# Optimization experiments

Hardware: AMD Instinct MI355X
Metric: run time of the kernel (lower is better)

Reference implementation:

```python
import jax, jax.numpy as jnp
import numpy as np

B, L, D = 32768, 256, 16  # batch, chain length, bond dim; physical dim d=2


def setup_inputs() -> dict:
    key = jax.random.key(0)
    k_phi, k_first, k_mid, k_last = jax.random.split(key, 4)
    scale = 1.0 / np.sqrt(2.0 * D)  # variance-preserving chain
    phi_batch = jax.random.normal(k_phi, (B, L, 2), dtype=jnp.float32)
    core_first = jax.random.normal(k_first, (2, D), dtype=jnp.float32) * scale
    cores_mid = jax.random.normal(k_mid, (L - 2, D, 2, D), dtype=jnp.float32) * scale
    core_last = jax.random.normal(k_last, (D, 2), dtype=jnp.float32) * scale
    out_bias = jnp.zeros((), dtype=jnp.float32)
    return {
        "phi_batch": phi_batch,
        "core_first": core_first,
        "cores_mid": cores_mid,
        "core_last": core_last,
        "out_bias": out_bias,
    }


def reference(phi_batch, core_first, cores_mid, core_last, out_bias):
    # MPS / tensor-train contraction, batched over samples.
    # Each sample contracts feature vectors phi[i] (len-2) into the physical
    # index of core i, then chains the resulting D x D matrices via a
    # left-to-right bond-space matvec (what cotengra would find per-sample).
    # v0: [B, D] = phi[:,0] contracted with first core [2, D]
    v0 = jnp.einsum("bp,pd->bd", phi_batch[:, 0], core_first)

    # middle features, scan-major layout: [L-2, B, 2]
    phis_mid = jnp.swapaxes(phi_batch[:, 1:-1], 0, 1)

    def step(v, xs):
        phi_t, core = xs  # phi_t: [B, 2], core: [D, 2, D]
        # contract bond then physical index; never materialize [B, D, D]
        u = jnp.einsum("bq,qpr->bpr", v, core)   # [B, 2, D]
        v_new = jnp.einsum("bp,bpr->br", phi_t, u)  # [B, D]
        return v_new, None

    v, _ = jax.lax.scan(step, v0, (phis_mid, cores_mid))

    # close the chain with last core [D, 2] and last feature [B, 2]
    out = jnp.einsum("bq,qp,bp->b", v, core_last, phi_batch[:, -1])
    return out + out_bias
```

## Files before the change

### kernel.cpp

```cpp
#include <hip/hip_runtime.h>
#include <stdint.h>


typedef short  bf16x8 __attribute__((ext_vector_type(8)));
typedef float  f32x4  __attribute__((ext_vector_type(4)));
typedef int    i32x4  __attribute__((ext_vector_type(4)));
typedef unsigned int u32;

#define NPF 64
#define NPB 63
#define BWD_OFF (NPF*4*64)

#define PACK_HI(hi, lo) ((int)__builtin_amdgcn_perm((u32)(hi), (u32)(lo), 0x07060302u))

__device__ __forceinline__ u32 rne_bump(u32 u){ return u + 0x7FFFu + ((u >> 16) & 1u); }

__global__ void build_pair_frags(const float* __restrict__ cm, i32x4* __restrict__ ws)
{
  __shared__ float Ca[512], Cb[512];
  const int bid = blockIdx.x;
  const bool fwd = bid < NPF;
  const int j  = fwd ? bid : bid - NPF;
  const int ta = fwd ? 2*j     : 252 - 2*j;
  const int tb = fwd ? 2*j + 1 : 253 - 2*j;
  {
    const float* A = cm + ta*512;
    const float* B = cm + tb*512;
    for (int i = threadIdx.x; i < 512; i += 256){ Ca[i] = A[i]; Cb[i] = B[i]; }
  }
  __syncthreads();
  const int f    = threadIdx.x >> 6;
  const int lane = threadIdx.x & 63;
  const int m    = lane & 15;
  const int g    = lane >> 4;
  const int p    = f >> 1, q = f & 1;
  u32 hi[4], lo[4];
  #pragma unroll
  for (int x = 0; x < 4; ++x){
    const int cq = 4*g + x;
    float acc = 0.f;
    #pragma unroll
    for (int r = 0; r < 16; ++r){
      const float a = fwd ? Ca[cq*32 + p*16 + r] : Ca[m*32 + p*16 + r];
      const float b = fwd ? Cb[r*32 + q*16 + m]  : Cb[r*32 + q*16 + cq];
      acc = fmaf(a, b, acc);
    }
    const u32 u  = __float_as_uint(acc);
    const u32 aa = rne_bump(u);
    const float hf = __uint_as_float(aa & 0xFFFF0000u);
    const u32 bb = rne_bump(__float_as_uint(acc - hf));
    hi[x] = aa >> 16; lo[x] = bb >> 16;
  }
  i32x4 w;
  w[0] = (int)(hi[0] | (hi[1] << 16));
  w[1] = (int)(hi[2] | (hi[3] << 16));
  w[2] = (int)(lo[0] | (lo[1] << 16));
  w[3] = (int)(lo[2] | (lo[3] << 16));
  ws[(fwd ? 0 : BWD_OFF) + (j*4 + f)*64 + lane] = w;
}

__device__ __forceinline__ void make_bfrag(const float (&v)[4], i32x4 &bfr)
{
  const u32 u0 = __float_as_uint(v[0]), u1 = __float_as_uint(v[1]);
  const u32 u2 = __float_as_uint(v[2]), u3 = __float_as_uint(v[3]);
  const float l0 = v[0] - __uint_as_float(u0 & 0xFFFF0000u);
  const float l1 = v[1] - __uint_as_float(u1 & 0xFFFF0000u);
  const float l2 = v[2] - __uint_as_float(u2 & 0xFFFF0000u);
  const float l3 = v[3] - __uint_as_float(u3 & 0xFFFF0000u);
  bfr[0] = PACK_HI(u1, u0);
  bfr[1] = PACK_HI(u3, u2);
  bfr[2] = PACK_HI(__float_as_uint(l1), __float_as_uint(l0));
  bfr[3] = PACK_HI(__float_as_uint(l3), __float_as_uint(l2));
}

__device__ __forceinline__ void pair_step(
    const i32x4 &G0, const i32x4 &G1, const i32x4 &G2, const i32x4 &G3,
    float2 cA, float2 cB, float (&v)[4], i32x4 &bfr)
{
  const float c00 = cA.x*cB.x, c01 = cA.x*cB.y;
  const float c10 = cA.y*cB.x, c11 = cA.y*cB.y;
  i32x4 sw; sw[0]=bfr[2]; sw[1]=bfr[3]; sw[2]=bfr[0]; sw[3]=bfr[1];
  const bf16x8 bh = __builtin_bit_cast(bf16x8, bfr);
  const bf16x8 bs = __builtin_bit_cast(bf16x8, sw);
  const f32x4 z = {0.f,0.f,0.f,0.f};
  f32x4 a00 = __builtin_amdgcn_mfma_f32_16x16x32_bf16(__builtin_bit_cast(bf16x8,G0), bh, z, 0,0,0);
  a00 = __builtin_amdgcn_mfma_f32_16x16x32_bf16(__builtin_bit_cast(bf16x8,G0), bs, a00, 0,0,0);
  f32x4 a01 = __builtin_amdgcn_mfma_f32_16x16x32_bf16(__builtin_bit_cast(bf16x8,G1), bh, z, 0,0,0);
  a01 = __builtin_amdgcn_mfma_f32_16x16x32_bf16(__builtin_bit_cast(bf16x8,G1), bs, a01, 0,0,0);
  f32x4 a10 = __builtin_amdgcn_mfma_f32_16x16x32_bf16(__builtin_bit_cast(bf16x8,G2), bh, z, 0,0,0);
  a10 = __builtin_amdgcn_mfma_f32_16x16x32_bf16(__builtin_bit_cast(bf16x8,G2), bs, a10, 0,0,0);
  f32x4 a11 = __builtin_amdgcn_mfma_f32_16x16x32_bf16(__builtin_bit_cast(bf16x8,G3), bh, z, 0,0,0);
  a11 = __builtin_amdgcn_mfma_f32_16x16x32_bf16(__builtin_bit_cast(bf16x8,G3), bs, a11, 0,0,0);
  #pragma unroll
  for (int i2 = 0; i2 < 4; ++i2)
    v[i2] = c00*a00[i2] + c01*a01[i2] + c10*a10[i2] + c11*a11[i2];
  make_bfrag(v, bfr);
}

__global__ __launch_bounds__(256, 2) void mps_chain(
  const float* __restrict__ phi,
  const float* __restrict__ core_first,
  const float* __restrict__ core_last,
  const float* __restrict__ bias,
  const i32x4* __restrict__ ws,
  float* __restrict__ out)
{
  const int lane = threadIdx.x & 63;
  const int wv   = threadIdx.x >> 6;
  const int n    = lane & 15;
  const int g    = lane >> 4;
  const bool isFwd = (wv < 2);
  const int dirIdx = isFwd ? 0 : 1;
  const int sb   = blockIdx.x * 64 + (wv & 1) * 32;

  __shared__ float red[128*20];

  const i32x4* wsD    = isFwd ? ws : (ws + BWD_OFF);
  const i32x4* wsLane = wsD + lane;

  const float*  row0 = phi + (size_t)(sb + n) * 512;
  const float*  row1 = phi + (size_t)(sb + 16 + n) * 512;
  const float2* c20  = (const float2*)row0;
  const float2* c21  = (const float2*)row1;

  const int uB = isFwd ? 1 : 253;
  const int vB = isFwd ? 3 : 251;
  const int st = isFwd ? 4 : -4;

  float vch[2][4];
  i32x4 bfr[2];
  {
    if (isFwd){
      const float2 p0 = *(const float2*)row0;
      const float2 p1 = *(const float2*)row1;
      #pragma unroll
      for (int r = 0; r < 4; ++r){
        const int rr = g*4 + r;
        vch[0][r] = p0.x * core_first[rr] + p0.y * core_first[16 + rr];
        vch[1][r] = p1.x * core_first[rr] + p1.y * core_first[16 + rr];
      }
    } else {
      const float2 p0 = *(const float2*)(row0 + 510);
      const float2 p1 = *(const float2*)(row1 + 510);
      #pragma unroll
      for (int r = 0; r < 4; ++r){
        const int rr = g*4 + r;
        vch[0][r] = p0.x * core_last[2*rr] + p0.y * core_last[2*rr + 1];
        vch[1][r] = p1.x * core_last[2*rr] + p1.y * core_last[2*rr + 1];
      }
    }
    make_bfrag(vch[0], bfr[0]);
    make_bfrag(vch[1], bfr[1]);
  }

  #pragma unroll 1
  for (int c = 0; c < 31; ++c){
    i32x4 A0,A1,A2,A3, B0,B1,B2,B3;
    { const i32x4* s = wsLane + (2*c    )*256; A0=s[0]; A1=s[64]; A2=s[128]; A3=s[192]; }
    { const i32x4* s = wsLane + (2*c + 1)*256; B0=s[0]; B1=s[64]; B2=s[128]; B3=s[192]; }
    const int u = uB + st*c, w = vB + st*c;
    const float2 eA0 = c20[u], eB0 = c20[u+1];
    const float2 eA1 = c21[u], eB1 = c21[u+1];
    const float2 oA0 = c20[w], oB0 = c20[w+1];
    const float2 oA1 = c21[w], oB1 = c21[w+1];

    pair_step(A0,A1,A2,A3, eA0,eB0, vch[0], bfr[0]);
    pair_step(A0,A1,A2,A3, eA1,eB1, vch[1], bfr[1]);
    pair_step(B0,B1,B2,B3, oA0,oB0, vch[0], bfr[0]);
    pair_step(B0,B1,B2,B3, oA1,oB1, vch[1], bfr[1]);
  }

  {
    i32x4 A0,A1,A2,A3, B0,B1,B2,B3;
    { const i32x4* s = wsLane + 62*256; A0=s[0]; A1=s[64]; A2=s[128]; A3=s[192]; }
    { const int j3 = isFwd ? 63 : 62;
      const i32x4* s = wsLane + j3*256; B0=s[0]; B1=s[64]; B2=s[128]; B3=s[192]; }
    const int u = uB + st*31, w = vB + st*31;
    const float2 eA0 = c20[u], eB0 = c20[u+1];
    const float2 eA1 = c21[u], eB1 = c21[u+1];
    const float2 oA0 = c20[w], oB0 = c20[w+1];
    const float2 oA1 = c21[w], oB1 = c21[w+1];

    pair_step(A0,A1,A2,A3, eA0,eB0, vch[0], bfr[0]);
    pair_step(A0,A1,A2,A3, eA1,eB1, vch[1], bfr[1]);
    if (isFwd){
      pair_step(B0,B1,B2,B3, oA0,oB0, vch[0], bfr[0]);
      pair_step(B0,B1,B2,B3, oA1,oB1, vch[1], bfr[1]);
    }
  }

  *(float4*)&red[(dirIdx*64 + (wv & 1)*32 + n)*20 + 4*g] =
      make_float4(vch[0][0], vch[0][1], vch[0][2], vch[0][3]);
  *(float4*)&red[(dirIdx*64 + (wv & 1)*32 + 16 + n)*20 + 4*g] =
      make_float4(vch[1][0], vch[1][1], vch[1][2], vch[1][3]);
  __syncthreads();
  if (threadIdx.x < 64){
    const int s = threadIdx.x;
    float acc = bias[0];
    #pragma unroll
    for (int qq = 0; qq < 16; ++qq)
      acc += red[s*20 + qq] * red[(64 + s)*20 + qq];
    out[blockIdx.x*64 + s] = acc;
  }
}

extern "C" void kernel_launch(void* const* d_in, const int* in_sizes, int n_in,
                              void* d_out, int out_size, void* d_ws, size_t ws_size,
                              hipStream_t stream)
{
  const float* phi  = (const float*)d_in[0];
  const float* cf   = (const float*)d_in[1];
  const float* cm   = (const float*)d_in[2];
  const float* cl   = (const float*)d_in[3];
  const float* bias = (const float*)d_in[4];
  i32x4* ws = (i32x4*)d_ws;

  build_pair_frags<<<NPF + NPB, 256, 0, stream>>>(cm, ws);
  mps_chain<<<512, 256, 0, stream>>>(phi, cf, cl, bias, ws, (float*)d_out);
}
```

Before: 148.8 us.

## Split chains one group per wave and software-prefetch pair fragments

Each wave now carries one 16-sample chain instead of two interleaved chains. The grid doubles to 1024 blocks and launch bounds rise to 4 blocks per CU, which adds occupancy. The main loop also prefetches the next pair's MFMA fragments and phi values while the current step runs, to hide global load latency. The cost is the loss of the ILP from two independent chains per wave, which made a serial MFMA dependency chain per wave. It also doubles the total fragment loads from the workspace.

```diff
diff --git a/kernel.cpp b/kernel.cpp
--- a/kernel.cpp
+++ b/kernel.cpp
@@ -97,7 +97,7 @@
   make_bfrag(v, bfr);
 }
 
-__global__ __launch_bounds__(256, 2) void mps_chain(
+__global__ __launch_bounds__(256, 4) void mps_chain(
   const float* __restrict__ phi,
   const float* __restrict__ core_first,
   const float* __restrict__ core_last,
@@ -107,100 +107,86 @@
 {
   const int lane = threadIdx.x & 63;
   const int wv   = threadIdx.x >> 6;
+  const int b0   = blockIdx.x * 32;
   const int n    = lane & 15;
   const int g    = lane >> 4;
+  const int half = wv & 1;
+  const int s_in = half*16 + n;
   const bool isFwd = (wv < 2);
   const int dirIdx = isFwd ? 0 : 1;
-  const int sb   = blockIdx.x * 64 + (wv & 1) * 32;
-
-  __shared__ float red[128*20];
+
+  __shared__ float red[64*20];
 
   const i32x4* wsD    = isFwd ? ws : (ws + BWD_OFF);
+  const int    maxPr  = isFwd ? NPF - 1 : NPB - 1;
   const i32x4* wsLane = wsD + lane;
 
-  const float*  row0 = phi + (size_t)(sb + n) * 512;
-  const float*  row1 = phi + (size_t)(sb + 16 + n) * 512;
-  const float2* c20  = (const float2*)row0;
-  const float2* c21  = (const float2*)row1;
+  const float*  row = phi + (size_t)(b0 + s_in) * 512;
+  const float2* c2  = (const float2*)row;
 
   const int uB = isFwd ? 1 : 253;
   const int vB = isFwd ? 3 : 251;
   const int st = isFwd ? 4 : -4;
 
-  float vch[2][4];
-  i32x4 bfr[2];
+  float v[4];
+  i32x4 bfr;
   {
     if (isFwd){
-      const float2 p0 = *(const float2*)row0;
-      const float2 p1 = *(const float2*)row1;
+      const float2 p0 = *(const float2*)row;
       #pragma unroll
       for (int r = 0; r < 4; ++r){
         const int rr = g*4 + r;
-        vch[0][r] = p0.x * core_first[rr] + p0.y * core_first[16 + rr];
-        vch[1][r] = p1.x * core_first[rr] + p1.y * core_first[16 + rr];
+        v[r] = p0.x * core_first[rr] + p0.y * core_first[16 + rr];
       }
     } else {
-      const float2 p0 = *(const float2*)(row0 + 510);
-      const float2 p1 = *(const float2*)(row1 + 510);
+      const float2 pL = *(const float2*)(row + 510);
       #pragma unroll
       for (int r = 0; r < 4; ++r){
         const int rr = g*4 + r;
-        vch[0][r] = p0.x * core_last[2*rr] + p0.y * core_last[2*rr + 1];
-        vch[1][r] = p1.x * core_last[2*rr] + p1.y * core_last[2*rr + 1];
+        v[r] = pL.x * core_last[2*rr] + pL.y * core_last[2*rr + 1];
       }
     }
-    make_bfrag(vch[0], bfr[0]);
-    make_bfrag(vch[1], bfr[1]);
-  }
+    make_bfrag(v, bfr);
+  }
+
+  i32x4 A0,A1,A2,A3, B0,B1,B2,B3;
+  float2 eA, eB, oA, oB;
+
+  { const i32x4* s = wsLane;        A0=s[0]; A1=s[64]; A2=s[128]; A3=s[192]; }
+  { const i32x4* s = wsLane + 256;  B0=s[0]; B1=s[64]; B2=s[128]; B3=s[192]; }
+  eA = c2[uB];     eB = c2[uB + 1];
+  oA = c2[vB];     oB = c2[vB + 1];
 
   #pragma unroll 1
   for (int c = 0; c < 31; ++c){
-    i32x4 A0,A1,A2,A3, B0,B1,B2,B3;
-    { const i32x4* s = wsLane + (2*c    )*256; A0=s[0]; A1=s[64]; A2=s[128]; A3=s[192]; }
-    { const i32x4* s = wsLane + (2*c + 1)*256; B0=s[0]; B1=s[64]; B2=s[128]; B3=s[192]; }
-    const int u = uB + st*c, w = vB + st*c;
-    const float2 eA0 = c20[u], eB0 = c20[u+1];
-    const float2 eA1 = c21[u], eB1 = c21[u+1];
-    const float2 oA0 = c20[w], oB0 = c20[w+1];
-    const float2 oA1 = c21[w], oB1 = c21[w+1];
-
-    pair_step(A0,A1,A2,A3, eA0,eB0, vch[0], bfr[0]);
-    pair_step(A0,A1,A2,A3, eA1,eB1, vch[1], bfr[1]);
-    pair_step(B0,B1,B2,B3, oA0,oB0, vch[0], bfr[0]);
-    pair_step(B0,B1,B2,B3, oA1,oB1, vch[1], bfr[1]);
-  }
-
-  {
-    i32x4 A0,A1,A2,A3, B0,B1,B2,B3;
-    { const i32x4* s = wsLane + 62*256; A0=s[0]; A1=s[64]; A2=s[128]; A3=s[192]; }
-    { const int j3 = isFwd ? 63 : 62;
-      const i32x4* s = wsLane + j3*256; B0=s[0]; B1=s[64]; B2=s[128]; B3=s[192]; }
-    const int u = uB + st*31, w = vB + st*31;
-    const float2 eA0 = c20[u], eB0 = c20[u+1];
-    const float2 eA1 = c21[u], eB1 = c21[u+1];
-    const float2 oA0 = c20[w], oB0 = c20[w+1];
-    const float2 oA1 = c21[w], oB1 = c21[w+1];
-
-    pair_step(A0,A1,A2,A3, eA0,eB0, vch[0], bfr[0]);
-    pair_step(A0,A1,A2,A3, eA1,eB1, vch[1], bfr[1]);
-    if (isFwd){
-      pair_step(B0,B1,B2,B3, oA0,oB0, vch[0], bfr[0]);
-      pair_step(B0,B1,B2,B3, oA1,oB1, vch[1], bfr[1]);
-    }
-  }
-
-  *(float4*)&red[(dirIdx*64 + (wv & 1)*32 + n)*20 + 4*g] =
-      make_float4(vch[0][0], vch[0][1], vch[0][2], vch[0][3]);
-  *(float4*)&red[(dirIdx*64 + (wv & 1)*32 + 16 + n)*20 + 4*g] =
-      make_float4(vch[1][0], vch[1][1], vch[1][2], vch[1][3]);
+    pair_step(A0,A1,A2,A3, eA,eB, v, bfr);
+    { const i32x4* s = wsLane + (2*c + 2)*256;
+      A0=s[0]; A1=s[64]; A2=s[128]; A3=s[192]; }
+
+    pair_step(B0,B1,B2,B3, oA,oB, v, bfr);
+    { int j3 = 2*c + 3; if (j3 > maxPr) j3 = maxPr;
+      const i32x4* s = wsLane + j3*256;
+      B0=s[0]; B1=s[64]; B2=s[128]; B3=s[192]; }
+
+    const int u1 = uB + st*(c+1), w1 = vB + st*(c+1);
+    eA = c2[u1]; eB = c2[u1+1];
+    oA = c2[w1]; oB = c2[w1+1];
+  }
+
+  pair_step(A0,A1,A2,A3, eA,eB, v, bfr);
+  if (isFwd)
+    pair_step(B0,B1,B2,B3, oA,oB, v, bfr);
+
+  *(float4*)&red[(dirIdx*32 + s_in)*20 + 4*g] =
+      make_float4(v[0], v[1], v[2], v[3]);
   __syncthreads();
-  if (threadIdx.x < 64){
+  if (threadIdx.x < 32){
     const int s = threadIdx.x;
     float acc = bias[0];
     #pragma unroll
     for (int qq = 0; qq < 16; ++qq)
-      acc += red[s*20 + qq] * red[(64 + s)*20 + qq];
-    out[blockIdx.x*64 + s] = acc;
+      acc += red[s*20 + qq] * red[(32 + s)*20 + qq];
+    out[b0 + s] = acc;
   }
 }
 
@@ -216,5 +202,5 @@
   i32x4* ws = (i32x4*)d_ws;
 
   build_pair_frags<<<NPF + NPB, 256, 0, stream>>>(cm, ws);
-  mps_chain<<<512, 256, 0, stream>>>(phi, cf, cl, bias, ws, (float*)d_out);
-}
+  mps_chain<<<1024, 256, 0, stream>>>(phi, cf, cl, bias, ws, (float*)d_out);
+}
```

After: 158.6 us. +6.6%, slower.
